# Kernel tuning notes

Measured on AMD Instinct MI355X. Metric: run time of the kernel, lower is better.

Reference implementation:

```python
import jax, jax.numpy as jnp
import numpy as np

SCALE = 4          # sigma // 2 with sigma = 8
EP = 1e-20         # epsilon used by xcorr_torch


def _pad(x, w):
    # zero-pad last two (spatial) dims by w on each side
    cfg = [(0, 0)] * (x.ndim - 2) + [(w, w), (w, w)]
    return jnp.pad(x, cfg)


def _box(x, w):
    # sliding 2w x 2w box sum via 2D integral image (cumsum trick),
    # matching xcorr_torch's cumsum/difference formulation.
    c = jnp.cumsum(jnp.cumsum(x, axis=-1), axis=-2)
    return (c[..., 2 * w:, 2 * w:] - c[..., :-2 * w, 2 * w:]
            - c[..., 2 * w:, :-2 * w] + c[..., :-2 * w, :-2 * w])


def _xcorr(a, b, w):
    # local (windowed) normalized cross-correlation field.
    # a: [B,C,1,H,W], b: [B,1,L,H,W]; broadcasting gives [B,C,L,H,W]
    a_mu = _box(_pad(a, w), w) / (4.0 * w * w)
    b_mu = _box(_pad(b, w), w) / (4.0 * w * w)
    ac = _pad(a - a_mu, w)
    bc = _pad(b - b_mu, w)
    sii = jnp.maximum(_box(ac * ac, w), EP)   # clip lower bound; upper clip at
    sjj = jnp.maximum(_box(bc * bc, w), EP)   # tensor max in torch is a no-op
    sij = _box(ac * bc, w)                    # [B,C,L,H,W]
    return sij / (jnp.sqrt(sii * sjj) + EP)


def setup_inputs() -> dict:
    key = jax.random.key(0)
    k1, k2 = jax.random.split(key)
    outputs = jax.random.uniform(k1, (4, 6, 512, 512), dtype=jnp.float32)
    labels = jax.random.uniform(k2, (4, 4, 512, 512), dtype=jnp.float32)
    return {"outputs": outputs, "labels": labels}


def reference(outputs, labels):
    w = SCALE
    a = outputs[:, :, None]            # [B,C,1,H,W]
    b = labels[:, None, :]             # [B,1,L,H,W]
    cc = _xcorr(a, b, w)               # [B,C,L,H,W] (torch loop over L, vectorized)
    Y = jnp.maximum(cc, -1.0)          # torch.clamp(min=-1)
    Y = jnp.max(Y, axis=2)             # amax over label channels -> [B,C,H,W]
    Y = jnp.clip(Y, -1.0, 1.0)
    X = 1.0 - Y
    return (jnp.mean(X), jnp.mean(X, axis=(2, 3)))
```

## Files before the change

### kernel.cpp

```cpp
#include <hip/hip_runtime.h>
#include <hip/hip_fp16.h>

#define HH 512
#define WW 512
#define HW (HH*WW)
#define EPV 1e-20f


__device__ __forceinline__ float bpl(int addr, float v) {
    return __int_as_float(__builtin_amdgcn_ds_bpermute(addr, __float_as_int(v)));
}
__device__ __forceinline__ int rcl(int r) { return min(max(r, 0), HH - 1); }

__device__ __forceinline__ float4 h2f4(uint2 r) {
    __half2 lo = *(__half2*)&r.x, hi = *(__half2*)&r.y;
    float2 a = __half22float2(lo), b = __half22float2(hi);
    return make_float4(a.x, a.y, b.x, b.y);
}
__device__ __forceinline__ uint2 f2h4(float4 v) {
    __half2 lo = __floats2half2_rn(v.x, v.y);
    __half2 hi = __floats2half2_rn(v.z, v.w);
    uint2 r;
    r.x = *(unsigned int*)&lo;
    r.y = *(unsigned int*)&hi;
    return r;
}
__device__ __forceinline__ uint4 pack8(float4 a, float4 b) {
    uint2 lo = f2h4(a), hi = f2h4(b);
    return make_uint4(lo.x, lo.y, hi.x, hi.y);
}
__device__ __forceinline__ void unpack8(uint4 r, float4& a, float4& b) {
    a = h2f4(make_uint2(r.x, r.y));
    b = h2f4(make_uint2(r.z, r.w));
}

__global__ void __launch_bounds__(64)
__attribute__((amdgpu_waves_per_eu(3, 3)))
prep_f8(const float* __restrict__ outs, const float* __restrict__ labs,
        __half* __restrict__ ac, __half* __restrict__ rs,
        float* __restrict__ wsum)
{
    const int l = threadIdx.x;
    if (blockIdx.x == 0 && blockIdx.y == 0 && l < 24)
        wsum[l * 64] = 0.f;
    const int y0 = 8 * blockIdx.x;
    const int z  = blockIdx.y;

    const float* src = (z < 24) ? outs + z * HW : labs + (z - 24) * HW;
    __half* acd = ac + z * HW;
    __half* rsd = rs + z * HW;

    const int   col = 8 * l;
    const int   aL1 = ((l - 1) & 63) << 2;
    const int   aR1 = ((l + 1) & 63) << 2;
    const float lmE = (l > 0)  ? 1.f : 0.f;
    const float rmE = (l < 63) ? 1.f : 0.f;

    float4 fNA[2], fNB[2];
    float4 fOA[2], fOB[2];
    float4 fCA[2], fCB[2];
    uint4  pk[8];
    float4 VAa = {0,0,0,0}, VAb = {0,0,0,0};
    float4 Vqa = {0,0,0,0}, Vqb = {0,0,0,0};
    #pragma unroll
    for (int k = 0; k < 8; ++k) pk[k] = make_uint4(0,0,0,0);
    #pragma unroll
    for (int k = 0; k < 2; ++k) {
        fOA[k] = make_float4(0,0,0,0); fOB[k] = make_float4(0,0,0,0);
        fCA[k] = make_float4(0,0,0,0); fCB[k] = make_float4(0,0,0,0);
    }
    fNA[0] = *(const float4*)&src[rcl(y0 - 7) * WW + col];
    fNB[0] = *(const float4*)&src[rcl(y0 - 7) * WW + col + 4];
    fNA[1] = *(const float4*)&src[rcl(y0 - 6) * WW + col];
    fNB[1] = *(const float4*)&src[rcl(y0 - 6) * WW + col + 4];

    auto step = [&](const int t) {
        const int   r  = y0 - 7 + t;
        const float rm = (r >= 0 && r < HH) ? 1.f : 0.f;
        {
            float4 ra = fNA[t & 1], rb = fNB[t & 1];
            VAa.x += ra.x*rm; VAa.y += ra.y*rm; VAa.z += ra.z*rm; VAa.w += ra.w*rm;
            VAb.x += rb.x*rm; VAb.y += rb.y*rm; VAb.z += rb.z*rm; VAb.w += rb.w*rm;
        }
        if (t >= 8) {
            const float rm8 = ((r - 8) >= 0 && (r - 8) < HH) ? 1.f : 0.f;
            float4 oa = fOA[t & 1], ob = fOB[t & 1];
            VAa.x -= oa.x*rm8; VAa.y -= oa.y*rm8; VAa.z -= oa.z*rm8; VAa.w -= oa.w*rm8;
            VAb.x -= ob.x*rm8; VAb.y -= ob.y*rm8; VAb.z -= ob.z*rm8; VAb.w -= ob.w*rm8;
        }
        if (t <= 20) {
            const int rn = rcl(r + 2);
            fNA[t & 1] = *(const float4*)&src[rn * WW + col];
            fNB[t & 1] = *(const float4*)&src[rn * WW + col + 4];
        }
        if (t >= 6 && t <= 20) {
            const int ro = rcl(r - 6);
            fOA[t & 1] = *(const float4*)&src[ro * WW + col];
            fOB[t & 1] = *(const float4*)&src[ro * WW + col + 4];
        }
        if (t >= 6 && t <= 20) {
            const int rc = rcl(r - 2);
            fCA[t & 1] = *(const float4*)&src[rc * WW + col];
            fCB[t & 1] = *(const float4*)&src[rc * WW + col + 4];
        }
        if (t >= 8) {
            const int   c  = r - 4;
            const float cm = (c >= 0 && c < HH) ? 1.f : 0.f;
            float p1 = VAa.x, p2 = p1+VAa.y, p3 = p2+VAa.z, p4 = p3+VAa.w;
            float p5 = p4+VAb.x, p6 = p5+VAb.y, p7 = p6+VAb.z, tt = p7+VAb.w;
            float s1 = VAb.w, s2 = VAb.z+s1, s3 = VAb.y+s2;
            float L1 = bpl(aL1, s1)*lmE, L2 = bpl(aL1, s2)*lmE, L3 = bpl(aL1, s3)*lmE;
            float R1 = bpl(aR1, p1)*rmE, R2 = bpl(aR1, p2)*rmE;
            float R3 = bpl(aR1, p3)*rmE, R4 = bpl(aR1, p4)*rmE;
            float4 rc0 = fCA[t & 1], rc1 = fCB[t & 1];
            float4 aL4, aH4;
            aL4.x = (rc0.x - (L3+p5)    * (1.f/64.f)) * cm;
            aL4.y = (rc0.y - (L2+p6)    * (1.f/64.f)) * cm;
            aL4.z = (rc0.z - (L1+p7)    * (1.f/64.f)) * cm;
            aL4.w = (rc0.w - tt         * (1.f/64.f)) * cm;
            aH4.x = (rc1.x - (tt-p1+R1) * (1.f/64.f)) * cm;
            aH4.y = (rc1.y - (tt-p2+R2) * (1.f/64.f)) * cm;
            aH4.z = (rc1.z - (tt-p3+R3) * (1.f/64.f)) * cm;
            aH4.w = (rc1.w - (tt-p4+R4) * (1.f/64.f)) * cm;
            uint4 pkNew = pack8(aL4, aH4);
            if (t >= 11 && t <= 18)
                *(uint4*)&acd[c * WW + col] = pkNew;
            float4 qnL, qnH; unpack8(pkNew, qnL, qnH);
            Vqa.x += qnL.x*qnL.x; Vqa.y += qnL.y*qnL.y;
            Vqa.z += qnL.z*qnL.z; Vqa.w += qnL.w*qnL.w;
            Vqb.x += qnH.x*qnH.x; Vqb.y += qnH.y*qnH.y;
            Vqb.z += qnH.z*qnH.z; Vqb.w += qnH.w*qnH.w;
            if (t >= 16) {
                float4 oL, oH; unpack8(pk[t & 7], oL, oH);
                Vqa.x -= oL.x*oL.x; Vqa.y -= oL.y*oL.y;
                Vqa.z -= oL.z*oL.z; Vqa.w -= oL.w*oL.w;
                Vqb.x -= oH.x*oH.x; Vqb.y -= oH.y*oH.y;
                Vqb.z -= oH.z*oH.z; Vqb.w -= oH.w*oH.w;
            }
            pk[t & 7] = pkNew;
            if (t >= 15 && t <= 22) {
                const int y = c - 4;
                float q1 = Vqa.x, q2 = q1+Vqa.y, q3 = q2+Vqa.z, q4 = q3+Vqa.w;
                float q5 = q4+Vqb.x, q6 = q5+Vqb.y, q7 = q6+Vqb.z, qt = q7+Vqb.w;
                float z1 = Vqb.w, z2 = Vqb.z+z1, z3 = Vqb.y+z2;
                float Lq1 = bpl(aL1, z1)*lmE, Lq2 = bpl(aL1, z2)*lmE, Lq3 = bpl(aL1, z3)*lmE;
                float Rq1 = bpl(aR1, q1)*rmE, Rq2 = bpl(aR1, q2)*rmE;
                float Rq3 = bpl(aR1, q3)*rmE, Rq4 = bpl(aR1, q4)*rmE;
                float4 rL, rH;
                rL.x = fminf(__frsqrt_rn(fmaxf(Lq3+q5,    EPV)), 60000.f);
                rL.y = fminf(__frsqrt_rn(fmaxf(Lq2+q6,    EPV)), 60000.f);
                rL.z = fminf(__frsqrt_rn(fmaxf(Lq1+q7,    EPV)), 60000.f);
                rL.w = fminf(__frsqrt_rn(fmaxf(qt,        EPV)), 60000.f);
                rH.x = fminf(__frsqrt_rn(fmaxf(qt-q1+Rq1, EPV)), 60000.f);
                rH.y = fminf(__frsqrt_rn(fmaxf(qt-q2+Rq2, EPV)), 60000.f);
                rH.z = fminf(__frsqrt_rn(fmaxf(qt-q3+Rq3, EPV)), 60000.f);
                rH.w = fminf(__frsqrt_rn(fmaxf(qt-q4+Rq4, EPV)), 60000.f);
                *(uint4*)&rsd[y * WW + col] = pack8(rL, rH);
            }
        }
    };
    #pragma unroll
    for (int t = 0; t < 23; ++t) step(t);
}

__global__ void __launch_bounds__(64)
__attribute__((amdgpu_waves_per_eu(2, 2)))
ncc_f8(const __half* __restrict__ ac, const __half* __restrict__ rs,
       float* __restrict__ wsum)
{
    const int l   = threadIdx.x;
    const int n   = blockIdx.x;
    const int xcd = n & 7;
    const int p   = n >> 3;
    const int zq  = p >> 6;
    const int seg = p & 63;
    const int z   = 3 * xcd + zq;
    const int b   = z / 6;
    const int y0  = 8 * seg;

    const __half* acp = ac + z * HW;
    const __half* sip = rs + z * HW;
    const __half* bcp[4]; const __half* sjp[4];
    #pragma unroll
    for (int j = 0; j < 4; ++j) {
        bcp[j] = ac + (24 + b * 4 + j) * HW;
        sjp[j] = rs + (24 + b * 4 + j) * HW;
    }

    const int   col = 8 * l;
    const int   aL1 = ((l - 1) & 63) << 2;
    const int   aR1 = ((l + 1) & 63) << 2;
    const float lmE = (l > 0)  ? 1.f : 0.f;
    const float rmE = (l < 63) ? 1.f : 0.f;

    uint4 fa[2], fb[4][2];
    uint4 oA, oB[4];
    {
        const int r0 = rcl(y0 - 3), r1 = rcl(y0 - 2);
        fa[0] = *(const uint4*)&acp[r0 * WW + col];
        fa[1] = *(const uint4*)&acp[r1 * WW + col];
        #pragma unroll
        for (int j = 0; j < 4; ++j) {
            fb[j][0] = *(const uint4*)&bcp[j][r0 * WW + col];
            fb[j][1] = *(const uint4*)&bcp[j][r1 * WW + col];
            oB[j] = make_uint4(0,0,0,0);
        }
        oA = make_uint4(0,0,0,0);
    }

    float4 VpL[4], VpH[4];
    uint4 psiB[2], psjB[2][4];
    float4 xsL = make_float4(0,0,0,0), xsH = make_float4(0,0,0,0);
    #pragma unroll
    for (int j = 0; j < 4; ++j) {
        VpL[j] = make_float4(0,0,0,0); VpH[j] = make_float4(0,0,0,0);
        psjB[0][j] = make_uint4(0,0,0,0); psjB[1][j] = make_uint4(0,0,0,0);
    }
    psiB[0] = make_uint4(0,0,0,0); psiB[1] = make_uint4(0,0,0,0);

    auto step = [&](const int t) {
        const int   c  = y0 - 3 + t;
        const float rm = (c >= 0 && c < HH) ? 1.f : 0.f;
        uint4 ar = fa[t & 1];
        uint4 br0 = fb[0][t & 1], br1 = fb[1][t & 1];
        uint4 br2 = fb[2][t & 1], br3 = fb[3][t & 1];
        uint4 arO = oA;
        uint4 bo0 = oB[0], bo1 = oB[1], bo2 = oB[2], bo3 = oB[3];
        if (t <= 12) {
            const int rn = rcl(c + 2);
            fa[t & 1] = *(const uint4*)&acp[rn * WW + col];
            #pragma unroll
            for (int j = 0; j < 4; ++j)
                fb[j][t & 1] = *(const uint4*)&bcp[j][rn * WW + col];
        }
        if (t >= 7 && t <= 13) {
            const int ro = rcl(c - 7);
            oA = *(const uint4*)&acp[ro * WW + col];
            #pragma unroll
            for (int j = 0; j < 4; ++j)
                oB[j] = *(const uint4*)&bcp[j][ro * WW + col];
        }
        {
            float4 avL, avH; unpack8(ar, avL, avH);
            avL.x *= rm; avL.y *= rm; avL.z *= rm; avL.w *= rm;
            avH.x *= rm; avH.y *= rm; avH.z *= rm; avH.w *= rm;
            float4 bL, bH;
            unpack8(br0, bL, bH);
            VpL[0].x += avL.x*bL.x; VpL[0].y += avL.y*bL.y; VpL[0].z += avL.z*bL.z; VpL[0].w += avL.w*bL.w;
            VpH[0].x += avH.x*bH.x; VpH[0].y += avH.y*bH.y; VpH[0].z += avH.z*bH.z; VpH[0].w += avH.w*bH.w;
            unpack8(br1, bL, bH);
            VpL[1].x += avL.x*bL.x; VpL[1].y += avL.y*bL.y; VpL[1].z += avL.z*bL.z; VpL[1].w += avL.w*bL.w;
            VpH[1].x += avH.x*bH.x; VpH[1].y += avH.y*bH.y; VpH[1].z += avH.z*bH.z; VpH[1].w += avH.w*bH.w;
            unpack8(br2, bL, bH);
            VpL[2].x += avL.x*bL.x; VpL[2].y += avL.y*bL.y; VpL[2].z += avL.z*bL.z; VpL[2].w += avL.w*bL.w;
            VpH[2].x += avH.x*bH.x; VpH[2].y += avH.y*bH.y; VpH[2].z += avH.z*bH.z; VpH[2].w += avH.w*bH.w;
            unpack8(br3, bL, bH);
            VpL[3].x += avL.x*bL.x; VpL[3].y += avL.y*bL.y; VpL[3].z += avL.z*bL.z; VpL[3].w += avL.w*bL.w;
            VpH[3].x += avH.x*bH.x; VpH[3].y += avH.y*bH.y; VpH[3].z += avH.z*bH.z; VpH[3].w += avH.w*bH.w;
        }
        if (t >= 8) {
            const float rmO = ((c - 8) >= 0) ? 1.f : 0.f;
            float4 avL, avH; unpack8(arO, avL, avH);
            avL.x *= rmO; avL.y *= rmO; avL.z *= rmO; avL.w *= rmO;
            avH.x *= rmO; avH.y *= rmO; avH.z *= rmO; avH.w *= rmO;
            float4 bL, bH;
            unpack8(bo0, bL, bH);
            VpL[0].x -= avL.x*bL.x; VpL[0].y -= avL.y*bL.y; VpL[0].z -= avL.z*bL.z; VpL[0].w -= avL.w*bL.w;
            VpH[0].x -= avH.x*bH.x; VpH[0].y -= avH.y*bH.y; VpH[0].z -= avH.z*bH.z; VpH[0].w -= avH.w*bH.w;
            unpack8(bo1, bL, bH);
            VpL[1].x -= avL.x*bL.x; VpL[1].y -= avL.y*bL.y; VpL[1].z -= avL.z*bL.z; VpL[1].w -= avL.w*bL.w;
            VpH[1].x -= avH.x*bH.x; VpH[1].y -= avH.y*bH.y; VpH[1].z -= avH.z*bH.z; VpH[1].w -= avH.w*bH.w;
            unpack8(bo2, bL, bH);
            VpL[2].x -= avL.x*bL.x; VpL[2].y -= avL.y*bL.y; VpL[2].z -= avL.z*bL.z; VpL[2].w -= avL.w*bL.w;
            VpH[2].x -= avH.x*bH.x; VpH[2].y -= avH.y*bH.y; VpH[2].z -= avH.z*bH.z; VpH[2].w -= avH.w*bH.w;
            unpack8(bo3, bL, bH);
            VpL[3].x -= avL.x*bL.x; VpL[3].y -= avL.y*bL.y; VpL[3].z -= avL.z*bL.z; VpL[3].w -= avL.w*bL.w;
            VpH[3].x -= avH.x*bH.x; VpH[3].y -= avH.y*bH.y; VpH[3].z -= avH.z*bH.z; VpH[3].w -= avH.w*bH.w;
        }
        if (t >= 7 && t <= 14) {
            float4 pL, pH; unpack8(psiB[t & 1], pL, pH);
            float4 mmL = make_float4(-1,-1,-1,-1), mmH = make_float4(-1,-1,-1,-1);
            #pragma unroll
            for (int j = 0; j < 4; ++j) {
                float q1 = VpL[j].x, q2 = q1+VpL[j].y, q3 = q2+VpL[j].z, q4 = q3+VpL[j].w;
                float q5 = q4+VpH[j].x, q6 = q5+VpH[j].y, q7 = q6+VpH[j].z, q8 = q7+VpH[j].w;
                float s1 = VpH[j].w, s2 = VpH[j].z+s1, s3 = VpH[j].y+s2;
                float L1 = bpl(aL1, s1)*lmE, L2 = bpl(aL1, s2)*lmE, L3 = bpl(aL1, s3)*lmE;
                float R1 = bpl(aR1, q1)*rmE, R2 = bpl(aR1, q2)*rmE;
                float R3 = bpl(aR1, q3)*rmE, R4 = bpl(aR1, q4)*rmE;
                float4 sL, sH; unpack8(psjB[t & 1][j], sL, sH);
                mmL.x = fmaxf(mmL.x, (L3+q5)    * (pL.x*sL.x));
                mmL.y = fmaxf(mmL.y, (L2+q6)    * (pL.y*sL.y));
                mmL.z = fmaxf(mmL.z, (L1+q7)    * (pL.z*sL.z));
                mmL.w = fmaxf(mmL.w, q8         * (pL.w*sL.w));
                mmH.x = fmaxf(mmH.x, (q8-q1+R1) * (pH.x*sH.x));
                mmH.y = fmaxf(mmH.y, (q8-q2+R2) * (pH.y*sH.y));
                mmH.z = fmaxf(mmH.z, (q8-q3+R3) * (pH.z*sH.z));
                mmH.w = fmaxf(mmH.w, (q8-q4+R4) * (pH.w*sH.w));
            }
            xsL.x += 1.f - fminf(mmL.x, 1.f);
            xsL.y += 1.f - fminf(mmL.y, 1.f);
            xsL.z += 1.f - fminf(mmL.z, 1.f);
            xsL.w += 1.f - fminf(mmL.w, 1.f);
            xsH.x += 1.f - fminf(mmH.x, 1.f);
            xsH.y += 1.f - fminf(mmH.y, 1.f);
            xsH.z += 1.f - fminf(mmH.z, 1.f);
            xsH.w += 1.f - fminf(mmH.w, 1.f);
        }
        if (t >= 5 && t <= 12) {
            const int yn = min(y0 + t - 5, HH - 1);
            psiB[t & 1] = *(const uint4*)&sip[yn * WW + col];
            #pragma unroll
            for (int j = 0; j < 4; ++j)
                psjB[t & 1][j] = *(const uint4*)&sjp[j][yn * WW + col];
        }
    };
    #pragma unroll
    for (int t = 0; t < 15; ++t) step(t);

    float xt = xsL.x + xsL.y + xsL.z + xsL.w + xsH.x + xsH.y + xsH.z + xsH.w;
    #pragma unroll
    for (int off = 32; off > 0; off >>= 1) xt += __shfl_down(xt, off);
    if (l == 0) atomicAdd(&wsum[z * 64], xt);
}

__global__ void fin_f4(const float* __restrict__ wsum, float* __restrict__ out)
{
    const int l = threadIdx.x;
    float v = (l < 24) ? wsum[l * 64] : 0.f;
    if (l < 24) out[1 + l] = v * (1.f / (float)HW);
    #pragma unroll
    for (int off = 32; off > 0; off >>= 1) v += __shfl_down(v, off);
    if (l == 0) out[0] = v * (1.f / (24.f * (float)HW));
}

extern "C" void kernel_launch(void* const* d_in, const int* in_sizes, int n_in,
                              void* d_out, int out_size, void* d_ws, size_t ws_size,
                              hipStream_t stream) {
    const float* outs = (const float*)d_in[0];
    const float* labs = (const float*)d_in[1];
    float* out = (float*)d_out;
    float* ws  = (float*)d_ws;

    __half* acw  = (__half*)ws;
    __half* rsw  = (__half*)ws + 40 * HW;
    float*  wsum = ws + 40 * HW;

    prep_f8<<<dim3(64, 40), 64, 0, stream>>>(outs, labs, acw, rsw, wsum);
    ncc_f8<<<dim3(1536, 1, 1), 64, 0, stream>>>(acw, rsw, wsum);
    fin_f4<<<dim3(1, 1, 1), 64, 0, stream>>>(wsum, out);
}
```

Baseline: 131.8 us.

## Load each source row once into packed ring buffer; restructure xcorr pipeline

In the first kernel, each input row is now loaded from global memory once and kept in a 13-entry register ring buffer as packed fp16, instead of being loaded three times (new, old and center rows). In the second kernel, the 15-step unrolled loop becomes an 11-step schedule: the warm-up steps accumulate two rows each, and the steady-state steps fuse the add, subtract and emit work through helper lambdas. The goal is fewer redundant global loads and less loop overhead. In exchange, the ring buffer adds register pressure, and reading the window from fp16 copies changes numerical precision slightly.

```diff
diff --git a/kernel.cpp b/kernel.cpp
--- a/kernel.cpp
+++ b/kernel.cpp
@@ -56,52 +56,40 @@
     const float lmE = (l > 0)  ? 1.f : 0.f;
     const float rmE = (l < 63) ? 1.f : 0.f;
 
-    float4 fNA[2], fNB[2];
-    float4 fOA[2], fOB[2];
-    float4 fCA[2], fCB[2];
-    uint4  pk[8];
+    auto ldpack = [&](int row) {
+        float4 a = *(const float4*)&src[row * WW + col];
+        float4 b = *(const float4*)&src[row * WW + col + 4];
+        return pack8(a, b);
+    };
+
+    uint4 rg[13];
+    uint4 pk[8];
     float4 VAa = {0,0,0,0}, VAb = {0,0,0,0};
     float4 Vqa = {0,0,0,0}, Vqb = {0,0,0,0};
     #pragma unroll
+    for (int k = 0; k < 13; ++k) rg[k] = make_uint4(0,0,0,0);
+    #pragma unroll
     for (int k = 0; k < 8; ++k) pk[k] = make_uint4(0,0,0,0);
-    #pragma unroll
-    for (int k = 0; k < 2; ++k) {
-        fOA[k] = make_float4(0,0,0,0); fOB[k] = make_float4(0,0,0,0);
-        fCA[k] = make_float4(0,0,0,0); fCB[k] = make_float4(0,0,0,0);
-    }
-    fNA[0] = *(const float4*)&src[rcl(y0 - 7) * WW + col];
-    fNB[0] = *(const float4*)&src[rcl(y0 - 7) * WW + col + 4];
-    fNA[1] = *(const float4*)&src[rcl(y0 - 6) * WW + col];
-    fNB[1] = *(const float4*)&src[rcl(y0 - 6) * WW + col + 4];
+    rg[6] = ldpack(rcl(y0 - 7));
+    rg[7] = ldpack(rcl(y0 - 6));
+    rg[8] = ldpack(rcl(y0 - 5));
 
     auto step = [&](const int t) {
         const int   r  = y0 - 7 + t;
         const float rm = (r >= 0 && r < HH) ? 1.f : 0.f;
         {
-            float4 ra = fNA[t & 1], rb = fNB[t & 1];
+            float4 ra, rb; unpack8(rg[(t + 6) % 13], ra, rb);
             VAa.x += ra.x*rm; VAa.y += ra.y*rm; VAa.z += ra.z*rm; VAa.w += ra.w*rm;
             VAb.x += rb.x*rm; VAb.y += rb.y*rm; VAb.z += rb.z*rm; VAb.w += rb.w*rm;
         }
         if (t >= 8) {
-            const float rm8 = ((r - 8) >= 0 && (r - 8) < HH) ? 1.f : 0.f;
-            float4 oa = fOA[t & 1], ob = fOB[t & 1];
+            const float rm8 = ((r - 8) >= 0) ? 1.f : 0.f;
+            float4 oa, ob; unpack8(rg[(t + 11) % 13], oa, ob);
             VAa.x -= oa.x*rm8; VAa.y -= oa.y*rm8; VAa.z -= oa.z*rm8; VAa.w -= oa.w*rm8;
             VAb.x -= ob.x*rm8; VAb.y -= ob.y*rm8; VAb.z -= ob.z*rm8; VAb.w -= ob.w*rm8;
         }
-        if (t <= 20) {
-            const int rn = rcl(r + 2);
-            fNA[t & 1] = *(const float4*)&src[rn * WW + col];
-            fNB[t & 1] = *(const float4*)&src[rn * WW + col + 4];
-        }
-        if (t >= 6 && t <= 20) {
-            const int ro = rcl(r - 6);
-            fOA[t & 1] = *(const float4*)&src[ro * WW + col];
-            fOB[t & 1] = *(const float4*)&src[ro * WW + col + 4];
-        }
-        if (t >= 6 && t <= 20) {
-            const int rc = rcl(r - 2);
-            fCA[t & 1] = *(const float4*)&src[rc * WW + col];
-            fCB[t & 1] = *(const float4*)&src[rc * WW + col + 4];
+        if (t <= 19) {
+            rg[(t + 9) % 13] = ldpack(rcl(y0 - 4 + t));
         }
         if (t >= 8) {
             const int   c  = r - 4;
@@ -112,7 +100,7 @@
             float L1 = bpl(aL1, s1)*lmE, L2 = bpl(aL1, s2)*lmE, L3 = bpl(aL1, s3)*lmE;
             float R1 = bpl(aR1, p1)*rmE, R2 = bpl(aR1, p2)*rmE;
             float R3 = bpl(aR1, p3)*rmE, R4 = bpl(aR1, p4)*rmE;
-            float4 rc0 = fCA[t & 1], rc1 = fCB[t & 1];
+            float4 rc0, rc1; unpack8(rg[(t + 2) % 13], rc0, rc1);
             float4 aL4, aH4;
             aL4.x = (rc0.x - (L3+p5)    * (1.f/64.f)) * cm;
             aL4.y = (rc0.y - (L2+p6)    * (1.f/64.f)) * cm;
@@ -193,130 +181,150 @@
     const float lmE = (l > 0)  ? 1.f : 0.f;
     const float rmE = (l < 63) ? 1.f : 0.f;
 
+    auto lda = [&](const __half* ptr, int row) {
+        return *(const uint4*)&ptr[row * WW + col];
+    };
+
     uint4 fa[2], fb[4][2];
     uint4 oA, oB[4];
+    uint4 psiB[2], psjB[2][4];
+    float4 VpL[4], VpH[4];
+    float4 xsL = make_float4(0,0,0,0), xsH = make_float4(0,0,0,0);
     {
         const int r0 = rcl(y0 - 3), r1 = rcl(y0 - 2);
-        fa[0] = *(const uint4*)&acp[r0 * WW + col];
-        fa[1] = *(const uint4*)&acp[r1 * WW + col];
+        fa[0] = lda(acp, r0); fa[1] = lda(acp, r1);
         #pragma unroll
         for (int j = 0; j < 4; ++j) {
-            fb[j][0] = *(const uint4*)&bcp[j][r0 * WW + col];
-            fb[j][1] = *(const uint4*)&bcp[j][r1 * WW + col];
+            fb[j][0] = lda(bcp[j], r0); fb[j][1] = lda(bcp[j], r1);
             oB[j] = make_uint4(0,0,0,0);
+            psjB[0][j] = make_uint4(0,0,0,0); psjB[1][j] = make_uint4(0,0,0,0);
+            VpL[j] = make_float4(0,0,0,0); VpH[j] = make_float4(0,0,0,0);
         }
         oA = make_uint4(0,0,0,0);
+        psiB[0] = make_uint4(0,0,0,0); psiB[1] = make_uint4(0,0,0,0);
     }
 
-    float4 VpL[4], VpH[4];
-    uint4 psiB[2], psjB[2][4];
-    float4 xsL = make_float4(0,0,0,0), xsH = make_float4(0,0,0,0);
-    #pragma unroll
-    for (int j = 0; j < 4; ++j) {
-        VpL[j] = make_float4(0,0,0,0); VpH[j] = make_float4(0,0,0,0);
-        psjB[0][j] = make_uint4(0,0,0,0); psjB[1][j] = make_uint4(0,0,0,0);
+    auto accRow = [&](uint4 a, uint4 b0, uint4 b1, uint4 b2, uint4 b3, float m) {
+        float4 avL, avH; unpack8(a, avL, avH);
+        avL.x *= m; avL.y *= m; avL.z *= m; avL.w *= m;
+        avH.x *= m; avH.y *= m; avH.z *= m; avH.w *= m;
+        float4 bL, bH;
+        unpack8(b0, bL, bH);
+        VpL[0].x += avL.x*bL.x; VpL[0].y += avL.y*bL.y; VpL[0].z += avL.z*bL.z; VpL[0].w += avL.w*bL.w;
+        VpH[0].x += avH.x*bH.x; VpH[0].y += avH.y*bH.y; VpH[0].z += avH.z*bH.z; VpH[0].w += avH.w*bH.w;
+        unpack8(b1, bL, bH);
+        VpL[1].x += avL.x*bL.x; VpL[1].y += avL.y*bL.y; VpL[1].z += avL.z*bL.z; VpL[1].w += avL.w*bL.w;
+        VpH[1].x += avH.x*bH.x; VpH[1].y += avH.y*bH.y; VpH[1].z += avH.z*bH.z; VpH[1].w += avH.w*bH.w;
+        unpack8(b2, bL, bH);
+        VpL[2].x += avL.x*bL.x; VpL[2].y += avL.y*bL.y; VpL[2].z += avL.z*bL.z; VpL[2].w += avL.w*bL.w;
+        VpH[2].x += avH.x*bH.x; VpH[2].y += avH.y*bH.y; VpH[2].z += avH.z*bH.z; VpH[2].w += avH.w*bH.w;
+        unpack8(b3, bL, bH);
+        VpL[3].x += avL.x*bL.x; VpL[3].y += avL.y*bL.y; VpL[3].z += avL.z*bL.z; VpL[3].w += avL.w*bL.w;
+        VpH[3].x += avH.x*bH.x; VpH[3].y += avH.y*bH.y; VpH[3].z += avH.z*bH.z; VpH[3].w += avH.w*bH.w;
+    };
+    auto emitRow = [&](uint4 cPsi, const uint4* cPsj) {
+        float4 pL, pH; unpack8(cPsi, pL, pH);
+        float4 mmL = make_float4(-1,-1,-1,-1), mmH = make_float4(-1,-1,-1,-1);
+        #pragma unroll
+        for (int j = 0; j < 4; ++j) {
+            float q1 = VpL[j].x, q2 = q1+VpL[j].y, q3 = q2+VpL[j].z, q4 = q3+VpL[j].w;
+            float q5 = q4+VpH[j].x, q6 = q5+VpH[j].y, q7 = q6+VpH[j].z, q8 = q7+VpH[j].w;
+            float s1 = VpH[j].w, s2 = VpH[j].z+s1, s3 = VpH[j].y+s2;
+            float L1 = bpl(aL1, s1)*lmE, L2 = bpl(aL1, s2)*lmE, L3 = bpl(aL1, s3)*lmE;
+            float R1 = bpl(aR1, q1)*rmE, R2 = bpl(aR1, q2)*rmE;
+            float R3 = bpl(aR1, q3)*rmE, R4 = bpl(aR1, q4)*rmE;
+            float4 sL, sH; unpack8(cPsj[j], sL, sH);
+            mmL.x = fmaxf(mmL.x, (L3+q5)    * (pL.x*sL.x));
+            mmL.y = fmaxf(mmL.y, (L2+q6)    * (pL.y*sL.y));
+            mmL.z = fmaxf(mmL.z, (L1+q7)    * (pL.z*sL.z));
+            mmL.w = fmaxf(mmL.w, q8         * (pL.w*sL.w));
+            mmH.x = fmaxf(mmH.x, (q8-q1+R1) * (pH.x*sH.x));
+            mmH.y = fmaxf(mmH.y, (q8-q2+R2) * (pH.y*sH.y));
+            mmH.z = fmaxf(mmH.z, (q8-q3+R3) * (pH.z*sH.z));
+            mmH.w = fmaxf(mmH.w, (q8-q4+R4) * (pH.w*sH.w));
+        }
+        xsL.x += 1.f - fminf(mmL.x, 1.f);
+        xsL.y += 1.f - fminf(mmL.y, 1.f);
+        xsL.z += 1.f - fminf(mmL.z, 1.f);
+        xsL.w += 1.f - fminf(mmL.w, 1.f);
+        xsH.x += 1.f - fminf(mmH.x, 1.f);
+        xsH.y += 1.f - fminf(mmH.y, 1.f);
+        xsH.z += 1.f - fminf(mmH.z, 1.f);
+        xsH.w += 1.f - fminf(mmH.w, 1.f);
+    };
+
+    #pragma unroll
+    for (int t = 0; t < 11; ++t) {
+        uint4 cPsi = psiB[t & 1];
+        uint4 cPsj[4] = { psjB[t & 1][0], psjB[t & 1][1],
+                          psjB[t & 1][2], psjB[t & 1][3] };
+        if (t <= 3) {
+            const int w0 = y0 - 3 + 2 * t;
+            uint4 a0 = fa[0], a1 = fa[1];
+            uint4 b00 = fb[0][0], b10 = fb[1][0], b20 = fb[2][0], b30 = fb[3][0];
+            uint4 b01 = fb[0][1], b11 = fb[1][1], b21 = fb[2][1], b31 = fb[3][1];
+            if (t <= 2) {
+                const int n0 = rcl(w0 + 2), n1 = rcl(w0 + 3);
+                fa[0] = lda(acp, n0); fa[1] = lda(acp, n1);
+                #pragma unroll
+                for (int j = 0; j < 4; ++j) {
+                    fb[j][0] = lda(bcp[j], n0); fb[j][1] = lda(bcp[j], n1);
+                }
+            } else {
+                const int n0 = rcl(y0 + 5), n1 = rcl(y0 + 6);
+                fa[0] = lda(acp, n0); fa[1] = lda(acp, n1);
+                #pragma unroll
+                for (int j = 0; j < 4; ++j) {
+                    fb[j][0] = lda(bcp[j], n0); fb[j][1] = lda(bcp[j], n1);
+                }
+                const int ro = rcl(y0 - 3);
+                oA = lda(acp, ro);
+                #pragma unroll
+                for (int j = 0; j < 4; ++j) oB[j] = lda(bcp[j], ro);
+            }
+            const float m0 = (w0     >= 0) ? 1.f : 0.f;
+            const float m1 = (w0 + 1 >= 0) ? 1.f : 0.f;
+            accRow(a0, b00, b10, b20, b30, m0);
+            accRow(a1, b01, b11, b21, b31, m1);
+            if (t >= 1) {
+                const int yn = y0 + t - 1;
+                psiB[t & 1] = lda(sip, yn);
+                #pragma unroll
+                for (int j = 0; j < 4; ++j) psjB[t & 1][j] = lda(sjp[j], yn);
+            }
+            if (t == 3) emitRow(cPsi, cPsj);
+        } else {
+            const int cadd = y0 + t + 1;
+            uint4 ar = fa[t & 1];
+            uint4 br0 = fb[0][t & 1], br1 = fb[1][t & 1];
+            uint4 br2 = fb[2][t & 1], br3 = fb[3][t & 1];
+            uint4 arO = oA;
+            uint4 bo0 = oB[0], bo1 = oB[1], bo2 = oB[2], bo3 = oB[3];
+            if (t <= 8) {
+                const int rn = rcl(cadd + 2);
+                fa[t & 1] = lda(acp, rn);
+                #pragma unroll
+                for (int j = 0; j < 4; ++j) fb[j][t & 1] = lda(bcp[j], rn);
+            }
+            if (t <= 9) {
+                const int ro = rcl(y0 + t - 6);
+                oA = lda(acp, ro);
+                #pragma unroll
+                for (int j = 0; j < 4; ++j) oB[j] = lda(bcp[j], ro);
+            }
+            if (t <= 8) {
+                const int yn = y0 + t - 1;
+                psiB[t & 1] = lda(sip, yn);
+                #pragma unroll
+                for (int j = 0; j < 4; ++j) psjB[t & 1][j] = lda(sjp[j], yn);
+            }
+            const float mA = (cadd < HH) ? 1.f : 0.f;
+            accRow(ar, br0, br1, br2, br3, mA);
+            const float mO = ((y0 + t - 7) >= 0) ? -1.f : 0.f;
+            accRow(arO, bo0, bo1, bo2, bo3, mO);
+            emitRow(cPsi, cPsj);
+        }
     }
-    psiB[0] = make_uint4(0,0,0,0); psiB[1] = make_uint4(0,0,0,0);
-
-    auto step = [&](const int t) {
-        const int   c  = y0 - 3 + t;
-        const float rm = (c >= 0 && c < HH) ? 1.f : 0.f;
-        uint4 ar = fa[t & 1];
-        uint4 br0 = fb[0][t & 1], br1 = fb[1][t & 1];
-        uint4 br2 = fb[2][t & 1], br3 = fb[3][t & 1];
-        uint4 arO = oA;
-        uint4 bo0 = oB[0], bo1 = oB[1], bo2 = oB[2], bo3 = oB[3];
-        if (t <= 12) {
-            const int rn = rcl(c + 2);
-            fa[t & 1] = *(const uint4*)&acp[rn * WW + col];
-            #pragma unroll
-            for (int j = 0; j < 4; ++j)
-                fb[j][t & 1] = *(const uint4*)&bcp[j][rn * WW + col];
-        }
-        if (t >= 7 && t <= 13) {
-            const int ro = rcl(c - 7);
-            oA = *(const uint4*)&acp[ro * WW + col];
-            #pragma unroll
-            for (int j = 0; j < 4; ++j)
-                oB[j] = *(const uint4*)&bcp[j][ro * WW + col];
-        }
-        {
-            float4 avL, avH; unpack8(ar, avL, avH);
-            avL.x *= rm; avL.y *= rm; avL.z *= rm; avL.w *= rm;
-            avH.x *= rm; avH.y *= rm; avH.z *= rm; avH.w *= rm;
-            float4 bL, bH;
-            unpack8(br0, bL, bH);
-            VpL[0].x += avL.x*bL.x; VpL[0].y += avL.y*bL.y; VpL[0].z += avL.z*bL.z; VpL[0].w += avL.w*bL.w;
-            VpH[0].x += avH.x*bH.x; VpH[0].y += avH.y*bH.y; VpH[0].z += avH.z*bH.z; VpH[0].w += avH.w*bH.w;
-            unpack8(br1, bL, bH);
-            VpL[1].x += avL.x*bL.x; VpL[1].y += avL.y*bL.y; VpL[1].z += avL.z*bL.z; VpL[1].w += avL.w*bL.w;
-            VpH[1].x += avH.x*bH.x; VpH[1].y += avH.y*bH.y; VpH[1].z += avH.z*bH.z; VpH[1].w += avH.w*bH.w;
-            unpack8(br2, bL, bH);
-            VpL[2].x += avL.x*bL.x; VpL[2].y += avL.y*bL.y; VpL[2].z += avL.z*bL.z; VpL[2].w += avL.w*bL.w;
-            VpH[2].x += avH.x*bH.x; VpH[2].y += avH.y*bH.y; VpH[2].z += avH.z*bH.z; VpH[2].w += avH.w*bH.w;
-            unpack8(br3, bL, bH);
-            VpL[3].x += avL.x*bL.x; VpL[3].y += avL.y*bL.y; VpL[3].z += avL.z*bL.z; VpL[3].w += avL.w*bL.w;
-            VpH[3].x += avH.x*bH.x; VpH[3].y += avH.y*bH.y; VpH[3].z += avH.z*bH.z; VpH[3].w += avH.w*bH.w;
-        }
-        if (t >= 8) {
-            const float rmO = ((c - 8) >= 0) ? 1.f : 0.f;
-            float4 avL, avH; unpack8(arO, avL, avH);
-            avL.x *= rmO; avL.y *= rmO; avL.z *= rmO; avL.w *= rmO;
-            avH.x *= rmO; avH.y *= rmO; avH.z *= rmO; avH.w *= rmO;
-            float4 bL, bH;
-            unpack8(bo0, bL, bH);
-            VpL[0].x -= avL.x*bL.x; VpL[0].y -= avL.y*bL.y; VpL[0].z -= avL.z*bL.z; VpL[0].w -= avL.w*bL.w;
-            VpH[0].x -= avH.x*bH.x; VpH[0].y -= avH.y*bH.y; VpH[0].z -= avH.z*bH.z; VpH[0].w -= avH.w*bH.w;
-            unpack8(bo1, bL, bH);
-            VpL[1].x -= avL.x*bL.x; VpL[1].y -= avL.y*bL.y; VpL[1].z -= avL.z*bL.z; VpL[1].w -= avL.w*bL.w;
-            VpH[1].x -= avH.x*bH.x; VpH[1].y -= avH.y*bH.y; VpH[1].z -= avH.z*bH.z; VpH[1].w -= avH.w*bH.w;
-            unpack8(bo2, bL, bH);
-            VpL[2].x -= avL.x*bL.x; VpL[2].y -= avL.y*bL.y; VpL[2].z -= avL.z*bL.z; VpL[2].w -= avL.w*bL.w;
-            VpH[2].x -= avH.x*bH.x; VpH[2].y -= avH.y*bH.y; VpH[2].z -= avH.z*bH.z; VpH[2].w -= avH.w*bH.w;
-            unpack8(bo3, bL, bH);
-            VpL[3].x -= avL.x*bL.x; VpL[3].y -= avL.y*bL.y; VpL[3].z -= avL.z*bL.z; VpL[3].w -= avL.w*bL.w;
-            VpH[3].x -= avH.x*bH.x; VpH[3].y -= avH.y*bH.y; VpH[3].z -= avH.z*bH.z; VpH[3].w -= avH.w*bH.w;
-        }
-        if (t >= 7 && t <= 14) {
-            float4 pL, pH; unpack8(psiB[t & 1], pL, pH);
-            float4 mmL = make_float4(-1,-1,-1,-1), mmH = make_float4(-1,-1,-1,-1);
-            #pragma unroll
-            for (int j = 0; j < 4; ++j) {
-                float q1 = VpL[j].x, q2 = q1+VpL[j].y, q3 = q2+VpL[j].z, q4 = q3+VpL[j].w;
-                float q5 = q4+VpH[j].x, q6 = q5+VpH[j].y, q7 = q6+VpH[j].z, q8 = q7+VpH[j].w;
-                float s1 = VpH[j].w, s2 = VpH[j].z+s1, s3 = VpH[j].y+s2;
-                float L1 = bpl(aL1, s1)*lmE, L2 = bpl(aL1, s2)*lmE, L3 = bpl(aL1, s3)*lmE;
-                float R1 = bpl(aR1, q1)*rmE, R2 = bpl(aR1, q2)*rmE;
-                float R3 = bpl(aR1, q3)*rmE, R4 = bpl(aR1, q4)*rmE;
-                float4 sL, sH; unpack8(psjB[t & 1][j], sL, sH);
-                mmL.x = fmaxf(mmL.x, (L3+q5)    * (pL.x*sL.x));
-                mmL.y = fmaxf(mmL.y, (L2+q6)    * (pL.y*sL.y));
-                mmL.z = fmaxf(mmL.z, (L1+q7)    * (pL.z*sL.z));
-                mmL.w = fmaxf(mmL.w, q8         * (pL.w*sL.w));
-                mmH.x = fmaxf(mmH.x, (q8-q1+R1) * (pH.x*sH.x));
-                mmH.y = fmaxf(mmH.y, (q8-q2+R2) * (pH.y*sH.y));
-                mmH.z = fmaxf(mmH.z, (q8-q3+R3) * (pH.z*sH.z));
-                mmH.w = fmaxf(mmH.w, (q8-q4+R4) * (pH.w*sH.w));
-            }
-            xsL.x += 1.f - fminf(mmL.x, 1.f);
-            xsL.y += 1.f - fminf(mmL.y, 1.f);
-            xsL.z += 1.f - fminf(mmL.z, 1.f);
-            xsL.w += 1.f - fminf(mmL.w, 1.f);
-            xsH.x += 1.f - fminf(mmH.x, 1.f);
-            xsH.y += 1.f - fminf(mmH.y, 1.f);
-            xsH.z += 1.f - fminf(mmH.z, 1.f);
-            xsH.w += 1.f - fminf(mmH.w, 1.f);
-        }
-        if (t >= 5 && t <= 12) {
-            const int yn = min(y0 + t - 5, HH - 1);
-            psiB[t & 1] = *(const uint4*)&sip[yn * WW + col];
-            #pragma unroll
-            for (int j = 0; j < 4; ++j)
-                psjB[t & 1][j] = *(const uint4*)&sjp[j][yn * WW + col];
-        }
-    };
-    #pragma unroll
-    for (int t = 0; t < 15; ++t) step(t);
 
     float xt = xsL.x + xsL.y + xsL.z + xsL.w + xsH.x + xsH.y + xsH.z + xsH.w;
     #pragma unroll
```

New measurement: 161.9 us. 22.9% more time.
